# Optimization experiments

Hardware: AMD Instinct MI355X
Metric: run time of the kernel (lower is better)

## Reference

```python
import jax, jax.numpy as jnp
import numpy as np

B, CIN, L = 256, 4, 8192
NF = 8          # num_init_features
UC = 16         # up_channel / inter_channels
EPS = 1e-5


def conv1d(x, w, b=None, padding=0, dilation=1):
    # x: (B, Cin, L), w: (Cout, Cin, K)
    out = jax.lax.conv_general_dilated(
        x, w, window_strides=(1,), padding=[(padding, padding)],
        rhs_dilation=(dilation,), dimension_numbers=('NCH', 'OIH', 'NCH'))
    if b is not None:
        out = out + b[None, :, None]
    return out


def bn_relu(x, gamma, beta, mean, var):
    # eval-mode BatchNorm1d followed by ReLU
    inv = gamma / jnp.sqrt(var + EPS)
    return jax.nn.relu((x - mean[None, :, None]) * inv[None, :, None]
                       + beta[None, :, None])


def setup_inputs() -> dict:
    key = jax.random.key(0)
    ks = jax.random.split(key, 16)
    sc = lambda *s: 0.05
    inp = {
        'x':   jax.random.normal(ks[0], (B, CIN, L), jnp.float32),
        'w00': jax.random.normal(ks[1], (NF, CIN, 32), jnp.float32) * 0.1,
        'b00': jax.random.normal(ks[2], (NF,), jnp.float32) * 0.1,
        'w01': jax.random.normal(ks[3], (NF, NF, 16), jnp.float32) * 0.1,
        'b01': jax.random.normal(ks[4], (NF,), jnp.float32) * 0.1,
        'w02': jax.random.normal(ks[5], (NF, NF, 16), jnp.float32) * 0.1,
        'b02': jax.random.normal(ks[6], (NF,), jnp.float32) * 0.1,
        'wc1': jax.random.normal(ks[7], (UC, CIN, 1), jnp.float32) * 0.1,
        'g1':  jnp.ones((UC,), jnp.float32),
        'bt1': jnp.zeros((UC,), jnp.float32),
        'm1':  jax.random.normal(ks[8], (UC,), jnp.float32) * 0.1,
        'v1':  jax.random.uniform(ks[9], (UC,), jnp.float32, 0.5, 1.5),
        'beta_cam': jnp.full((1,), 0.5, jnp.float32),
        'wc2': jax.random.normal(ks[10], (UC, UC, 1), jnp.float32) * 0.1,
        'g2':  jnp.ones((UC,), jnp.float32),
        'bt2': jnp.zeros((UC,), jnp.float32),
        'm2':  jax.random.normal(ks[11], (UC,), jnp.float32) * 0.1,
        'v2':  jax.random.uniform(ks[12], (UC,), jnp.float32, 0.5, 1.5),
    }
    return inp


def channel_attention(x, beta_cam):
    # x: (B, C, L); attention over channels (C x C)
    attn = jnp.einsum('bcl,bdl->bcd', x, x)                      # (B,C,C)
    attn = jnp.max(attn, axis=-1, keepdims=True) - attn          # max-subtract
    attn = jax.nn.softmax(attn, axis=-1)
    feat_e = jnp.einsum('bcd,bdl->bcl', attn, x)
    return beta_cam * feat_e + x


def reference(x, w00, b00, w01, b01, w02, b02, wc1, g1, bt1, m1, v1,
              beta_cam, wc2, g2, bt2, m2, v2):
    # ConvFusion branch
    fea0 = conv1d(x, w00, b00, padding=16)                 # (B,8,L+1)
    fea1 = conv1d(fea0, w01, b01, padding=7)               # (B,8,L)
    fea2 = conv1d(fea0, w02, b02, padding=13, dilation=2)  # (B,8,L-3)
    fea2 = jnp.pad(fea2, ((0, 0), (0, 0), (1, 2)))         # (B,8,L)
    conv_fusion = jnp.concatenate([fea1, fea2], axis=1)    # (B,16,L)
    # Channel-attention branch
    c0 = bn_relu(conv1d(x, wc1), g1, bt1, m1, v1)          # (B,16,L)
    c1 = channel_attention(c0, beta_cam)
    c2 = bn_relu(conv1d(c1, wc2), g2, bt2, m2, v2)
    return conv_fusion + c2
```

## Files before the change

kernel.cpp:

```cpp
#include <hip/hip_runtime.h>

#define LL 8192

typedef __attribute__((ext_vector_type(8))) short bf16x8;
typedef __attribute__((ext_vector_type(4))) float f32x4;

union U4 { uint4 u; bf16x8 v; };

__device__ __forceinline__ unsigned short f2bf(float f) {
    union { float f; unsigned u; } v; v.f = f;
    unsigned r = v.u + 0x7fffu + ((v.u >> 16) & 1u);
    return (unsigned short)(r >> 16);
}
__device__ __forceinline__ unsigned cvt_pk_bf16(float lo, float hi) {
    unsigned r;
    asm("v_cvt_pk_bf16_f32 %0, %1, %2" : "=v"(r) : "v"(lo), "v"(hi));
    return r;
}

__global__ __launch_bounds__(256) void kernA1(
    const float* __restrict__ x, const float* __restrict__ wc1,
    const float* __restrict__ g1, const float* __restrict__ bt1,
    const float* __restrict__ m1, const float* __restrict__ v1,
    float* __restrict__ partial)
{
    __shared__ float xs[4][1024];
    __shared__ __align__(16) unsigned short c0f[16384];
    __shared__ float wf1[16][4];
    __shared__ float bf1[16];

    const int blk = blockIdx.x;
    const int b = blk >> 3, chunk = blk & 7;
    const int t = threadIdx.x;
    const int w = t >> 6, l = t & 63;
    const float* xb = x + (size_t)b * 4 * LL;
    const int p0 = chunk << 10;

    if (t < 16) {
        float inv = g1[t] * rsqrtf(v1[t] + 1e-5f);
        #pragma unroll
        for (int c = 0; c < 4; ++c) wf1[t][c] = wc1[t * 4 + c] * inv;
        bf1[t] = bt1[t] - m1[t] * inv;
    }
    #pragma unroll
    for (int c = 0; c < 4; ++c)
        for (int j = t; j < 1024; j += 256)
            xs[c][j] = xb[c * LL + p0 + j];
    __syncthreads();

    {
        const int u = t & 15, pblk = t >> 4;
        float w0 = wf1[u][0], w1 = wf1[u][1], w2 = wf1[u][2], w3 = wf1[u][3];
        float bu = bf1[u];
        #pragma unroll 4
        for (int pp = 0; pp < 64; pp += 2) {
            int p = (pblk << 6) + pp;
            float c00 = fmaxf(bu + w0 * xs[0][p] + w1 * xs[1][p]
                                 + w2 * xs[2][p] + w3 * xs[3][p], 0.f);
            float c01 = fmaxf(bu + w0 * xs[0][p + 1] + w1 * xs[1][p + 1]
                                 + w2 * xs[2][p + 1] + w3 * xs[3][p + 1], 0.f);
            int slot = ((p >> 5) << 6) + (((p >> 3) & 3) << 4) + u;
            *reinterpret_cast<unsigned*>(&c0f[slot * 8 + (p & 7)]) =
                cvt_pk_bf16(c00, c01);
        }
    }
    __syncthreads();

    f32x4 acc = {0.f, 0.f, 0.f, 0.f};
    #pragma unroll
    for (int m = 0; m < 8; ++m) {
        int slot = (w * 8 + m) * 64 + l;
        bf16x8 fr = *reinterpret_cast<const bf16x8*>(&c0f[slot * 8]);
        acc = __builtin_amdgcn_mfma_f32_16x16x32_bf16(fr, fr, acc, 0, 0, 0);
    }

    float* gsumf = &xs[0][0];
    {
        int col = l & 15, rg = l >> 4;
        #pragma unroll
        for (int i = 0; i < 4; ++i)
            gsumf[w * 256 + (rg * 4 + i) * 16 + col] = acc[i];
    }
    __syncthreads();
    partial[(size_t)(b * 8 + chunk) * 256 + t] =
        gsumf[t] + gsumf[256 + t] + gsumf[512 + t] + gsumf[768 + t];
}

__global__ __launch_bounds__(256) void kernA2(
    const float* __restrict__ partial, const float* __restrict__ beta_cam,
    const float* __restrict__ wc2, const float* __restrict__ g2,
    const float* __restrict__ bt2, const float* __restrict__ m2,
    const float* __restrict__ v2,
    const float* __restrict__ w00, const float* __restrict__ w01,
    const float* __restrict__ w02,
    const float* __restrict__ wc1, const float* __restrict__ g1,
    const float* __restrict__ bt1, const float* __restrict__ m1,
    const float* __restrict__ v1,
    unsigned short* __restrict__ Mp,
    unsigned short* __restrict__ wA0, unsigned short* __restrict__ wA1,
    unsigned short* __restrict__ wc0A)
{
    __shared__ float gram[16][16];
    __shared__ float attn[16][16];
    __shared__ float Msh[16][16];
    const int b = blockIdx.x, t = threadIdx.x;

    if (b == 0) {
        for (int i = t; i < 384; i += 256) {
            const int c = i >> 6, li = i & 63;
            const int row = li & 15, g = li >> 4;
            #pragma unroll
            for (int j = 0; j < 8; ++j) {
                int ch = j & 3;
                int T = 8 * c + g + ((j >= 4) ? 4 : 0);
                float v = 0.f;
                if (row < 8) {
                    if (T < 32) v = w00[(row * 4 + ch) * 32 + T];
                } else {
                    int tt = T - 16;
                    if (tt >= 0) v = w00[((row - 8) * 4 + ch) * 32 + tt];
                }
                wA0[(c * 64 + li) * 8 + j] = f2bf(v);
            }
            int q = (c == 0) ? 2 * g : (c == 5) ? 24 + 2 * g : 3 + 4 * c + g;
            #pragma unroll
            for (int j = 0; j < 8; ++j) {
                float v = 0.f;
                if (row < 8) {
                    if (q >= 7 && q <= 22) v = w01[(row * 8 + j) * 16 + (q - 7)];
                } else {
                    if (!(q & 1)) v = w02[((row - 8) * 8 + j) * 16 + (q >> 1)];
                }
                wA1[(c * 64 + li) * 8 + j] = f2bf(v);
            }
        }
        if (t < 64) {
            int u = t & 15, gg = t >> 4;
            float inv = g1[u] * rsqrtf(v1[u] + 1e-5f);
            #pragma unroll
            for (int j = 0; j < 8; ++j) {
                float v = 0.f;
                if (gg == 0) {
                    if (j < 4) v = wc1[u * 4 + j] * inv;
                    else if (j == 4) v = bt1[u] - m1[u] * inv;
                }
                wc0A[t * 8 + j] = f2bf(v);
            }
        }
    }

    const float* P = partial + (size_t)b * 2048;
    float s = 0.f;
    #pragma unroll
    for (int k = 0; k < 8; ++k) s += P[k * 256 + t];
    gram[t >> 4][t & 15] = s;
    __syncthreads();
    {
        const float beta = beta_cam[0];
        int d = t & 15;
        float gv = gram[t >> 4][d];
        float rm = gv;
        #pragma unroll
        for (int m = 1; m < 16; m <<= 1) rm = fmaxf(rm, __shfl_xor(rm, m, 64));
        float a = rm - gv;
        float am = a;
        #pragma unroll
        for (int m = 1; m < 16; m <<= 1) am = fmaxf(am, __shfl_xor(am, m, 64));
        float e = __expf(a - am);
        float ssum = e;
        #pragma unroll
        for (int m = 1; m < 16; m <<= 1) ssum += __shfl_xor(ssum, m, 64);
        attn[t >> 4][d] = beta * e / ssum;
    }
    __syncthreads();
    {
        int o = t >> 4, u = t & 15;
        float inv2 = g2[o] * rsqrtf(v2[o] + 1e-5f);
        float sm = wc2[o * 16 + u];
        #pragma unroll
        for (int d = 0; d < 16; ++d) sm += wc2[o * 16 + d] * attn[d][u];
        Msh[o][u] = sm * inv2;
    }
    __syncthreads();
    for (int idx = t; idx < 512; idx += 256) {
        int li = idx >> 3, j = idx & 7;
        int k = 8 * (li >> 4) + j, o = li & 15;
        float v = (k < 16) ? Msh[o][k] : 0.f;
        Mp[(size_t)b * 512 + idx] = f2bf(v);
    }
}

__global__ __launch_bounds__(256, 4) void kernB(
    const float* __restrict__ x,
    const float* __restrict__ b00, const float* __restrict__ b01,
    const float* __restrict__ b02,
    const float* __restrict__ g2, const float* __restrict__ bt2,
    const float* __restrict__ m2, const float* __restrict__ v2,
    const unsigned short* __restrict__ wA0, const unsigned short* __restrict__ wA1,
    const unsigned short* __restrict__ wc0A,
    const unsigned short* __restrict__ Mp, float* __restrict__ out)
{
    __shared__ __align__(16) unsigned short xT[608][8];
    __shared__ __align__(16) unsigned short f0T[576][8];

    const int blk = blockIdx.x;
    const int b  = blk >> 4;
    const int p0 = (blk & 15) << 9;
    const int t  = threadIdx.x;
    const int w  = t >> 6, l = t & 63;
    const int lane15 = l & 15, g = l >> 4;
    const float* xb = x + (size_t)b * 4 * LL;

    for (int i = t; i < 608; i += 256) {
        int xp = p0 - 32 + i;
        bool ok = (unsigned)xp < 8192u;
        float v0  = ok ? xb[0 * LL + xp] : 0.f;
        float v1_ = ok ? xb[1 * LL + xp] : 0.f;
        float v2_ = ok ? xb[2 * LL + xp] : 0.f;
        float v3_ = ok ? xb[3 * LL + xp] : 0.f;
        uint2 r;
        r.x = cvt_pk_bf16(v0, v1_);
        r.y = cvt_pk_bf16(v2_, v3_);
        *reinterpret_cast<uint2*>(&xT[i][0]) = r;
        if (i >= 4)
            *reinterpret_cast<uint2*>(&xT[i - 4][4]) = r;
    }

    bf16x8 a0[6];
    #pragma unroll
    for (int c = 0; c < 6; ++c)
        a0[c] = reinterpret_cast<const bf16x8*>(wA0)[c * 64 + l];
    float b00c[4];
    #pragma unroll
    for (int i = 0; i < 4; ++i) b00c[i] = b00[(4 * g + i) & 7];

    __syncthreads();

    {
        const int ngrp = (w < 2) ? 5 : 4;
        const int grp0 = (w < 2) ? 5 * w : 10 + 4 * (w - 2);
        const int rb = 32 * grp0 + lane15 + g;
        bf16x8 bb[6];
        #pragma unroll
        for (int c = 0; c < 6; ++c)
            bb[c] = *reinterpret_cast<const bf16x8*>(&xT[rb + 8 * c][0]);
        #pragma unroll
        for (int it = 0; it < 5; ++it) {
            if (it < ngrp) {
                f32x4 d = {0.f, 0.f, 0.f, 0.f};
                #pragma unroll
                for (int c = 0; c < 6; ++c)
                    d = __builtin_amdgcn_mfma_f32_16x16x32_bf16(a0[c], bb[c], d, 0, 0, 0);
                int s = 32 * (grp0 + it) + lane15 + ((g >= 2) ? 16 : 0);
                int j = p0 - 16 + s;
                bool ok = (unsigned)j <= 8192u;
                float e0 = ok ? d[0] + b00c[0] : 0.f;
                float e1 = ok ? d[1] + b00c[1] : 0.f;
                float e2 = ok ? d[2] + b00c[2] : 0.f;
                float e3 = ok ? d[3] + b00c[3] : 0.f;
                uint2 wv;
                wv.x = cvt_pk_bf16(e0, e1);
                wv.y = cvt_pk_bf16(e2, e3);
                *reinterpret_cast<uint2*>(&f0T[s][4 * (g & 1)]) = wv;
                if (it + 1 < ngrp) {
                    bb[0] = bb[4]; bb[1] = bb[5];
                    int nb = rb + 32 * (it + 1);
                    #pragma unroll
                    for (int c = 2; c < 6; ++c)
                        bb[c] = *reinterpret_cast<const bf16x8*>(&xT[nb + 8 * c][0]);
                }
            }
        }
    }

    bf16x8 a1[6];
    #pragma unroll
    for (int c = 0; c < 6; ++c)
        a1[c] = reinterpret_cast<const bf16x8*>(wA1)[c * 64 + l];
    bf16x8 mfrag  = reinterpret_cast<const bf16x8*>(Mp)[b * 64 + l];
    bf16x8 wc0Af  = reinterpret_cast<const bf16x8*>(wc0A)[l];
    float cb1[4], bf2v[4];
    #pragma unroll
    for (int i = 0; i < 4; ++i) {
        int o = 4 * g + i;
        cb1[i] = (o < 8) ? b01[o] : b02[o - 8];
        float inv2 = g2[o] * rsqrtf(v2[o] + 1e-5f);
        bf2v[i] = bt2[o] - m2[o] * inv2;
    }
    int qoff[6];
    qoff[0] = 2 * g + 2;  qoff[1] = 9 + g;   qoff[2] = 13 + g;
    qoff[3] = 17 + g;     qoff[4] = 21 + g;  qoff[5] = 26 + 2 * g;
    const int s0 = (lane15 + 32 * g) & 63;
    const int s1 = (s0 + 16) & 63;

    __syncthreads();

    {
        float* ob = out + (size_t)b * 16 * LL;
        const f32x4 zc = {0.f, 0.f, 0.f, 0.f};
        #pragma unroll
        for (int it = 0; it < 8; ++it) {
            const int gi = 8 * w + it;
            const int rbase = 16 * gi + lane15;
            bf16x8 bb[6];
            #pragma unroll
            for (int c = 0; c < 6; ++c)
                bb[c] = *reinterpret_cast<const bf16x8*>(&f0T[rbase + qoff[c]][0]);
            f32x4 dF = {0.f, 0.f, 0.f, 0.f};
            #pragma unroll
            for (int c = 0; c < 6; ++c)
                dF = __builtin_amdgcn_mfma_f32_16x16x32_bf16(a1[c], bb[c], dF, 0, 0, 0);

            U4 xu; xu.u.x = 0u; xu.u.y = 0u; xu.u.z = 0u; xu.u.w = 0u;
            if (g == 0) {
                uint2 xr = *reinterpret_cast<const uint2*>(&xT[rbase + 32][0]);
                xu.u.x = xr.x; xu.u.y = xr.y;
                xu.u.z = 0x3f80u;
            }
            f32x4 dP = __builtin_amdgcn_mfma_f32_16x16x32_bf16(wc0Af, xu.v, zc, 0, 0, 0);
            unsigned pk0 = cvt_pk_bf16(fmaxf(dP[0], 0.f), fmaxf(dP[1], 0.f));
            unsigned pk1 = cvt_pk_bf16(fmaxf(dP[2], 0.f), fmaxf(dP[3], 0.f));
            U4 uu;
            uu.u.x = __shfl(pk0, s0, 64);
            uu.u.y = __shfl(pk1, s0, 64);
            uu.u.z = __shfl(pk0, s1, 64);
            uu.u.w = __shfl(pk1, s1, 64);
            f32x4 dC = __builtin_amdgcn_mfma_f32_16x16x32_bf16(mfrag, uu.v, zc, 0, 0, 0);

            const int p = p0 + 16 * gi + lane15;
            const bool edge = (p < 1) | (p > LL - 3);
            float* op = ob + p;
            #pragma unroll
            for (int i = 0; i < 4; ++i) {
                int o = 4 * g + i;
                float vf = dF[i] + cb1[i];
                if (o >= 8 && edge) vf = 0.f;
                float c2 = fmaxf(dC[i] + bf2v[i], 0.f);
                op[(size_t)o * LL] = vf + c2;
            }
        }
    }
}

extern "C" void kernel_launch(void* const* d_in, const int* in_sizes, int n_in,
                              void* d_out, int out_size, void* d_ws, size_t ws_size,
                              hipStream_t stream)
{
    const float* x    = (const float*)d_in[0];
    const float* w00  = (const float*)d_in[1];
    const float* b00  = (const float*)d_in[2];
    const float* w01  = (const float*)d_in[3];
    const float* b01  = (const float*)d_in[4];
    const float* w02  = (const float*)d_in[5];
    const float* b02  = (const float*)d_in[6];
    const float* wc1  = (const float*)d_in[7];
    const float* g1   = (const float*)d_in[8];
    const float* bt1  = (const float*)d_in[9];
    const float* m1   = (const float*)d_in[10];
    const float* v1   = (const float*)d_in[11];
    const float* beta = (const float*)d_in[12];
    const float* wc2  = (const float*)d_in[13];
    const float* g2   = (const float*)d_in[14];
    const float* bt2  = (const float*)d_in[15];
    const float* m2   = (const float*)d_in[16];
    const float* v2   = (const float*)d_in[17];

    char* wsb = (char*)d_ws;
    float* partialp       = (float*)wsb;
    unsigned short* Mpp   = (unsigned short*)(wsb + 2097152);
    unsigned short* wA0p  = (unsigned short*)(wsb + 2359296);
    unsigned short* wA1p  = (unsigned short*)(wsb + 2365440);
    unsigned short* wc0Ap = (unsigned short*)(wsb + 2371584);
    float* o = (float*)d_out;

    hipLaunchKernelGGL(kernA1, dim3(2048), dim3(256), 0, stream,
        x, wc1, g1, bt1, m1, v1, partialp);
    hipLaunchKernelGGL(kernA2, dim3(256), dim3(256), 0, stream,
        partialp, beta, wc2, g2, bt2, m2, v2, w00, w01, w02,
        wc1, g1, bt1, m1, v1, Mpp, wA0p, wA1p, wc0Ap);
    hipLaunchKernelGGL(kernB, dim3(4096), dim3(256), 0, stream,
        x, b00, b01, b02, g2, bt2, m2, v2,
        wA0p, wA1p, wc0Ap, Mpp, o);
}
```

Measured before the change: 81.13 us.

## Restructure conv MFMA loops with sliding B-fragment reuse and interior-block fast paths

The second conv stage is restructured to use 8 uniformly spaced K-chunks, with the weight matrix repacked to 512 entries and the workspace offset moved to fit it. This lets B fragments slide between iterations so only half are reloaded from LDS each step. Biases are folded into the MFMA accumulator initialisation. Interior blocks skip the boundary masking on both load and store, and kernA1 loads x with float4. The trade-off is two more MFMAs per iteration on zero-padded weights, plus some extra registers.

```diff
diff --git a/kernel.cpp b/kernel.cpp
--- a/kernel.cpp
+++ b/kernel.cpp
@@ -7,6 +7,9 @@
 
 union U4 { uint4 u; bf16x8 v; };
 
+__device__ __forceinline__ float4 ld4(const float* p) {
+    return *reinterpret_cast<const float4*>(p);
+}
 __device__ __forceinline__ unsigned short f2bf(float f) {
     union { float f; unsigned u; } v; v.f = f;
     unsigned r = v.u + 0x7fffu + ((v.u >> 16) & 1u);
@@ -43,9 +46,10 @@
         bf1[t] = bt1[t] - m1[t] * inv;
     }
     #pragma unroll
-    for (int c = 0; c < 4; ++c)
-        for (int j = t; j < 1024; j += 256)
-            xs[c][j] = xb[c * LL + p0 + j];
+    for (int c = 0; c < 4; ++c) {
+        float4 v = ld4(&xb[c * LL + p0 + 4 * t]);
+        *reinterpret_cast<float4*>(&xs[c][4 * t]) = v;
+    }
     __syncthreads();
 
     {
@@ -122,7 +126,11 @@
                 }
                 wA0[(c * 64 + li) * 8 + j] = f2bf(v);
             }
-            int q = (c == 0) ? 2 * g : (c == 5) ? 24 + 2 * g : 3 + 4 * c + g;
+        }
+        for (int i = t; i < 512; i += 256) {
+            const int c = i >> 6, li = i & 63;
+            const int row = li & 15, g = li >> 4;
+            int q = 4 * c + g;
             #pragma unroll
             for (int j = 0; j < 8; ++j) {
                 float v = 0.f;
@@ -210,20 +218,37 @@
     const int w  = t >> 6, l = t & 63;
     const int lane15 = l & 15, g = l >> 4;
     const float* xb = x + (size_t)b * 4 * LL;
-
-    for (int i = t; i < 608; i += 256) {
-        int xp = p0 - 32 + i;
-        bool ok = (unsigned)xp < 8192u;
-        float v0  = ok ? xb[0 * LL + xp] : 0.f;
-        float v1_ = ok ? xb[1 * LL + xp] : 0.f;
-        float v2_ = ok ? xb[2 * LL + xp] : 0.f;
-        float v3_ = ok ? xb[3 * LL + xp] : 0.f;
-        uint2 r;
-        r.x = cvt_pk_bf16(v0, v1_);
-        r.y = cvt_pk_bf16(v2_, v3_);
-        *reinterpret_cast<uint2*>(&xT[i][0]) = r;
-        if (i >= 4)
-            *reinterpret_cast<uint2*>(&xT[i - 4][4]) = r;
+    const bool intr = (p0 != 0) && (p0 != 15 * 512);
+
+    if (intr) {
+        for (int i = t; i < 608; i += 256) {
+            int xp = p0 - 32 + i;
+            float v0  = xb[0 * LL + xp];
+            float v1_ = xb[1 * LL + xp];
+            float v2_ = xb[2 * LL + xp];
+            float v3_ = xb[3 * LL + xp];
+            uint2 r;
+            r.x = cvt_pk_bf16(v0, v1_);
+            r.y = cvt_pk_bf16(v2_, v3_);
+            *reinterpret_cast<uint2*>(&xT[i][0]) = r;
+            if (i >= 4)
+                *reinterpret_cast<uint2*>(&xT[i - 4][4]) = r;
+        }
+    } else {
+        for (int i = t; i < 608; i += 256) {
+            int xp = p0 - 32 + i;
+            bool ok = (unsigned)xp < 8192u;
+            float v0  = ok ? xb[0 * LL + xp] : 0.f;
+            float v1_ = ok ? xb[1 * LL + xp] : 0.f;
+            float v2_ = ok ? xb[2 * LL + xp] : 0.f;
+            float v3_ = ok ? xb[3 * LL + xp] : 0.f;
+            uint2 r;
+            r.x = cvt_pk_bf16(v0, v1_);
+            r.y = cvt_pk_bf16(v2_, v3_);
+            *reinterpret_cast<uint2*>(&xT[i][0]) = r;
+            if (i >= 4)
+                *reinterpret_cast<uint2*>(&xT[i - 4][4]) = r;
+        }
     }
 
     bf16x8 a0[6];
@@ -239,43 +264,45 @@
     {
         const int ngrp = (w < 2) ? 5 : 4;
         const int grp0 = (w < 2) ? 5 * w : 10 + 4 * (w - 2);
-        const int rb = 32 * grp0 + lane15 + g;
+        const unsigned short* xrow = &xT[32 * grp0 + lane15 + g][0];
+        const int s_base = 32 * grp0 + lane15 + ((g >= 2) ? 16 : 0);
+        unsigned short* wp = &f0T[s_base][4 * (g & 1)];
         bf16x8 bb[6];
         #pragma unroll
         for (int c = 0; c < 6; ++c)
-            bb[c] = *reinterpret_cast<const bf16x8*>(&xT[rb + 8 * c][0]);
+            bb[c] = *reinterpret_cast<const bf16x8*>(xrow + 64 * c);
         #pragma unroll
         for (int it = 0; it < 5; ++it) {
             if (it < ngrp) {
-                f32x4 d = {0.f, 0.f, 0.f, 0.f};
+                f32x4 d = {b00c[0], b00c[1], b00c[2], b00c[3]};
                 #pragma unroll
                 for (int c = 0; c < 6; ++c)
                     d = __builtin_amdgcn_mfma_f32_16x16x32_bf16(a0[c], bb[c], d, 0, 0, 0);
-                int s = 32 * (grp0 + it) + lane15 + ((g >= 2) ? 16 : 0);
-                int j = p0 - 16 + s;
-                bool ok = (unsigned)j <= 8192u;
-                float e0 = ok ? d[0] + b00c[0] : 0.f;
-                float e1 = ok ? d[1] + b00c[1] : 0.f;
-                float e2 = ok ? d[2] + b00c[2] : 0.f;
-                float e3 = ok ? d[3] + b00c[3] : 0.f;
+                float e0 = d[0], e1 = d[1], e2 = d[2], e3 = d[3];
+                if (!intr) {
+                    int j = p0 - 16 + s_base + 32 * it;
+                    bool ok = (unsigned)j <= 8192u;
+                    e0 = ok ? e0 : 0.f;  e1 = ok ? e1 : 0.f;
+                    e2 = ok ? e2 : 0.f;  e3 = ok ? e3 : 0.f;
+                }
                 uint2 wv;
                 wv.x = cvt_pk_bf16(e0, e1);
                 wv.y = cvt_pk_bf16(e2, e3);
-                *reinterpret_cast<uint2*>(&f0T[s][4 * (g & 1)]) = wv;
+                *reinterpret_cast<uint2*>(wp + 256 * it) = wv;
                 if (it + 1 < ngrp) {
                     bb[0] = bb[4]; bb[1] = bb[5];
-                    int nb = rb + 32 * (it + 1);
                     #pragma unroll
                     for (int c = 2; c < 6; ++c)
-                        bb[c] = *reinterpret_cast<const bf16x8*>(&xT[nb + 8 * c][0]);
-                }
-            }
-        }
-    }
-
-    bf16x8 a1[6];
-    #pragma unroll
-    for (int c = 0; c < 6; ++c)
+                        bb[c] = *reinterpret_cast<const bf16x8*>(
+                            xrow + 32 * 8 * (it + 1) + 64 * c);
+                }
+            }
+        }
+    }
+
+    bf16x8 a1[8];
+    #pragma unroll
+    for (int c = 0; c < 8; ++c)
         a1[c] = reinterpret_cast<const bf16x8*>(wA1)[c * 64 + l];
     bf16x8 mfrag  = reinterpret_cast<const bf16x8*>(Mp)[b * 64 + l];
     bf16x8 wc0Af  = reinterpret_cast<const bf16x8*>(wc0A)[l];
@@ -287,36 +314,41 @@
         float inv2 = g2[o] * rsqrtf(v2[o] + 1e-5f);
         bf2v[i] = bt2[o] - m2[o] * inv2;
     }
-    int qoff[6];
-    qoff[0] = 2 * g + 2;  qoff[1] = 9 + g;   qoff[2] = 13 + g;
-    qoff[3] = 17 + g;     qoff[4] = 21 + g;  qoff[5] = 26 + 2 * g;
+    const unsigned mask1 = (g == 0) ? 0x3f80u : 0u;
+    const bool g0 = (g == 0);
     const int s0 = (lane15 + 32 * g) & 63;
     const int s1 = (s0 + 16) & 63;
 
     __syncthreads();
 
     {
-        float* ob = out + (size_t)b * 16 * LL;
+        const int gi0 = 8 * w;
+        const unsigned short* frow = &f0T[16 * gi0 + lane15 + g + 2][0];
+        const unsigned short* xrow2 = &xT[16 * gi0 + lane15 + 32][0];
+        const size_t obase = (size_t)b * 16 * LL + p0 + 16 * gi0 + lane15;
+        float* o0 = out + obase + (size_t)(4 * g + 0) * LL;
+        float* o1 = out + obase + (size_t)(4 * g + 1) * LL;
+        float* o2 = out + obase + (size_t)(4 * g + 2) * LL;
+        float* o3 = out + obase + (size_t)(4 * g + 3) * LL;
         const f32x4 zc = {0.f, 0.f, 0.f, 0.f};
+
+        bf16x8 bb[8];
+        #pragma unroll
+        for (int c = 0; c < 8; ++c)
+            bb[c] = *reinterpret_cast<const bf16x8*>(frow + 32 * c);
         #pragma unroll
         for (int it = 0; it < 8; ++it) {
-            const int gi = 8 * w + it;
-            const int rbase = 16 * gi + lane15;
-            bf16x8 bb[6];
+            f32x4 dF = {cb1[0], cb1[1], cb1[2], cb1[3]};
             #pragma unroll
-            for (int c = 0; c < 6; ++c)
-                bb[c] = *reinterpret_cast<const bf16x8*>(&f0T[rbase + qoff[c]][0]);
-            f32x4 dF = {0.f, 0.f, 0.f, 0.f};
-            #pragma unroll
-            for (int c = 0; c < 6; ++c)
+            for (int c = 0; c < 8; ++c)
                 dF = __builtin_amdgcn_mfma_f32_16x16x32_bf16(a1[c], bb[c], dF, 0, 0, 0);
 
-            U4 xu; xu.u.x = 0u; xu.u.y = 0u; xu.u.z = 0u; xu.u.w = 0u;
-            if (g == 0) {
-                uint2 xr = *reinterpret_cast<const uint2*>(&xT[rbase + 32][0]);
-                xu.u.x = xr.x; xu.u.y = xr.y;
-                xu.u.z = 0x3f80u;
-            }
+            uint2 xr = *reinterpret_cast<const uint2*>(xrow2 + 128 * it);
+            U4 xu;
+            xu.u.x = g0 ? xr.x : 0u;
+            xu.u.y = g0 ? xr.y : 0u;
+            xu.u.z = mask1;
+            xu.u.w = 0u;
             f32x4 dP = __builtin_amdgcn_mfma_f32_16x16x32_bf16(wc0Af, xu.v, zc, 0, 0, 0);
             unsigned pk0 = cvt_pk_bf16(fmaxf(dP[0], 0.f), fmaxf(dP[1], 0.f));
             unsigned pk1 = cvt_pk_bf16(fmaxf(dP[2], 0.f), fmaxf(dP[3], 0.f));
@@ -325,18 +357,30 @@
             uu.u.y = __shfl(pk1, s0, 64);
             uu.u.z = __shfl(pk0, s1, 64);
             uu.u.w = __shfl(pk1, s1, 64);
-            f32x4 dC = __builtin_amdgcn_mfma_f32_16x16x32_bf16(mfrag, uu.v, zc, 0, 0, 0);
-
-            const int p = p0 + 16 * gi + lane15;
-            const bool edge = (p < 1) | (p > LL - 3);
-            float* op = ob + p;
-            #pragma unroll
-            for (int i = 0; i < 4; ++i) {
-                int o = 4 * g + i;
-                float vf = dF[i] + cb1[i];
-                if (o >= 8 && edge) vf = 0.f;
-                float c2 = fmaxf(dC[i] + bf2v[i], 0.f);
-                op[(size_t)o * LL] = vf + c2;
+            f32x4 dC = {bf2v[0], bf2v[1], bf2v[2], bf2v[3]};
+            dC = __builtin_amdgcn_mfma_f32_16x16x32_bf16(mfrag, uu.v, dC, 0, 0, 0);
+
+            float c20 = fmaxf(dC[0], 0.f), c21 = fmaxf(dC[1], 0.f);
+            float c22 = fmaxf(dC[2], 0.f), c23 = fmaxf(dC[3], 0.f);
+            float r0 = dF[0] + c20, r1 = dF[1] + c21;
+            float r2 = dF[2] + c22, r3 = dF[3] + c23;
+            if (!intr) {
+                int p = p0 + 16 * (gi0 + it) + lane15;
+                if (((p < 1) | (p > LL - 3)) && g >= 2) {
+                    r0 = c20; r1 = c21; r2 = c22; r3 = c23;
+                }
+            }
+            o0[16 * it] = r0;
+            o1[16 * it] = r1;
+            o2[16 * it] = r2;
+            o3[16 * it] = r3;
+
+            if (it < 7) {
+                bb[0] = bb[4]; bb[1] = bb[5]; bb[2] = bb[6]; bb[3] = bb[7];
+                #pragma unroll
+                for (int c = 4; c < 8; ++c)
+                    bb[c] = *reinterpret_cast<const bf16x8*>(
+                        frow + 16 * 8 * (it + 1) + 32 * c);
             }
         }
     }
@@ -370,7 +414,7 @@
     unsigned short* Mpp   = (unsigned short*)(wsb + 2097152);
     unsigned short* wA0p  = (unsigned short*)(wsb + 2359296);
     unsigned short* wA1p  = (unsigned short*)(wsb + 2365440);
-    unsigned short* wc0Ap = (unsigned short*)(wsb + 2371584);
+    unsigned short* wc0Ap = (unsigned short*)(wsb + 2373632);
     float* o = (float*)d_out;
 
     hipLaunchKernelGGL(kernA1, dim3(2048), dim3(256), 0, stream,
```

Result: faster. 70.81 us (-12.7%).
